# Kernel optimization log

Measured on AMD Instinct MI355X. Metric: run time of the kernel, lower is better.

The kernel has to match this reference:

```python
import jax, jax.numpy as jnp
import numpy as np

EPS = 1e-5
N_NODES = 10
NUM_JOINTS = 6   # all robot_configs fixed to '3_segments_3DOF' (module's fallback default)
MAX_DOF = 10


def _lin(x, w, b):
    # torch nn.Linear: y = x @ W.T + b, W is (out, in)
    return jnp.einsum('...i,oi->...o', x, w) + b


def _layernorm(x, scale, bias):
    mu = x.mean(-1, keepdims=True)
    var = x.var(-1, keepdims=True)
    return (x - mu) / jnp.sqrt(var + EPS) * scale + bias


def _forward(images, text_lengths, node_features, edge_indices, p):
    B = images.shape[0]
    # --- SimplifiedVLMBackbone ---
    y = jax.lax.conv_general_dilated(images, p['conv_w'], (2, 2), [(3, 3), (3, 3)],
                                     dimension_numbers=('NCHW', 'OIHW', 'NCHW'))
    y = jax.nn.relu(y + p['conv_b'][None, :, None, None])          # (B,32,112,112)
    y = y.reshape(B, 32, 7, 16, 7, 16).mean(axis=(3, 5))            # adaptive avg pool -> (B,32,7,7)
    y = y.reshape(B, 32 * 49)
    y = jax.nn.relu(_lin(y, p['img_fc1_w'], p['img_fc1_b']))
    img_feat = _lin(y, p['img_fc2_w'], p['img_fc2_b'])               # (B,768)
    t = p['text_emb'][jnp.clip(text_lengths, 0, 9999)]               # (B,256)
    vlm = img_feat + _lin(t, p['text_fc_w'], p['text_fc_b'])         # (B,768)

    # --- SoftArmGraphNN ---
    x = jax.nn.relu(_lin(node_features, p['enc1_w'], p['enc1_b']))
    x = _lin(x, p['enc2_w'], p['enc2_b'])                            # (B,N,64)
    src, dst = edge_indices[:, 0, :], edge_indices[:, 1, :]          # (B,E)

    def agg_fn(xi, si, di):
        # mean of neighbor (source) features per destination node; 0 if no neighbors
        g = xi[si]                                                   # (E,D)
        s = jax.ops.segment_sum(g, di, num_segments=N_NODES)
        c = jax.ops.segment_sum(jnp.ones(di.shape, xi.dtype), di, num_segments=N_NODES)
        return s / jnp.maximum(c, 1.0)[:, None]

    for i in range(3):
        residual = x
        mean_nb = jax.vmap(agg_fn)(x, src, dst)                      # (B,N,64)
        comb = jnp.concatenate([x, mean_nb], axis=-1)                # (B,N,128)
        x = _lin(comb, p['gc_w'][i], p['gc_b'][i])
        x = jax.nn.relu(_layernorm(x + residual, p['ln_scale'][i], p['ln_bias'][i]))
    graph_tokens = _lin(x, p['proj_w'], p['proj_b'])                 # (B,N,32)

    # --- AttentionPooling + dual-path fusion ---
    s = _lin(jnp.tanh(_lin(graph_tokens, p['attn1_w'], p['attn1_b'])), p['attn2_w'], p['attn2_b'])
    w = jax.nn.softmax(s, axis=1)                                    # (B,N,1)
    robot_token = jnp.sum(graph_tokens * w, axis=1)                  # (B,32) -> project? 32 vs 768 -> residual add via broadcast pad
    fused = vlm.at[:, :robot_token.shape[-1]].add(robot_token)       # global token residual into vlm features

    # --- NodeActionHead (all samples: 3seg_3DOF -> 6 joints, per-joint MLPs) ---
    comb = jnp.concatenate([
        jnp.broadcast_to(fused[:, None, :], (B, NUM_JOINTS, fused.shape[-1])),
        graph_tokens[:, :NUM_JOINTS, :]], axis=-1)                   # (B,J,800)
    h = jax.nn.relu(jnp.einsum('bjf,jhf->bjh', comb, p['head_w1']) + p['head_b1'])
    h = jax.nn.relu(jnp.einsum('bjf,jhf->bjh', h, p['head_w2']) + p['head_b2'])
    a = jnp.einsum('bjf,jhf->bjh', h, p['head_w3']) + p['head_b3']   # (B,6,16)
    a = jnp.pad(a, ((0, 0), (0, MAX_DOF - NUM_JOINTS), (0, 0)))      # pad to max_dof
    return jnp.transpose(a, (0, 2, 1))                               # (B,16,10)


def setup_inputs() -> dict:
    key = jax.random.key(0)
    ks = iter(jax.random.split(key, 64))

    def nrm(shape, scale=0.02):
        return scale * jax.random.normal(next(ks), shape, dtype=jnp.float32)

    B = 128
    inp = {
        'images': jax.random.normal(next(ks), (B, 3, 224, 224), dtype=jnp.float32),
        'text_lengths': jax.random.randint(next(ks), (B,), 0, 10000, dtype=jnp.int32),
        'node_features': jax.random.normal(next(ks), (B, N_NODES, 19), dtype=jnp.float32),
        'edge_indices': jax.random.randint(next(ks), (B, 2, 18), 0, N_NODES, dtype=jnp.int32),
        'conv_w': nrm((32, 3, 7, 7)), 'conv_b': jnp.zeros(32, jnp.float32),
        'img_fc1_w': nrm((512, 1568)), 'img_fc1_b': jnp.zeros(512, jnp.float32),
        'img_fc2_w': nrm((768, 512)), 'img_fc2_b': jnp.zeros(768, jnp.float32),
        'text_emb': nrm((10000, 256)),
        'text_fc_w': nrm((768, 256)), 'text_fc_b': jnp.zeros(768, jnp.float32),
        'enc1_w': nrm((64, 19)), 'enc1_b': jnp.zeros(64, jnp.float32),
        'enc2_w': nrm((64, 64)), 'enc2_b': jnp.zeros(64, jnp.float32),
        'gc_w': nrm((3, 64, 128)), 'gc_b': jnp.zeros((3, 64), jnp.float32),
        'ln_scale': jnp.ones((3, 64), jnp.float32), 'ln_bias': jnp.zeros((3, 64), jnp.float32),
        'proj_w': nrm((32, 64)), 'proj_b': jnp.zeros(32, jnp.float32),
        'attn1_w': nrm((16, 32)), 'attn1_b': jnp.zeros(16, jnp.float32),
        'attn2_w': nrm((1, 16)), 'attn2_b': jnp.zeros(1, jnp.float32),
        'head_w1': nrm((6, 128, 800)), 'head_b1': jnp.zeros((6, 128), jnp.float32),
        'head_w2': nrm((6, 64, 128)), 'head_b2': jnp.zeros((6, 64), jnp.float32),
        'head_w3': nrm((6, 16, 64)), 'head_b3': jnp.zeros((6, 16), jnp.float32),
    }
    return inp


def reference(images, text_lengths, node_features, edge_indices, conv_w, conv_b,
              img_fc1_w, img_fc1_b, img_fc2_w, img_fc2_b, text_emb, text_fc_w, text_fc_b,
              enc1_w, enc1_b, enc2_w, enc2_b, gc_w, gc_b, ln_scale, ln_bias,
              proj_w, proj_b, attn1_w, attn1_b, attn2_w, attn2_b,
              head_w1, head_b1, head_w2, head_b2, head_w3, head_b3):
    p = dict(conv_w=conv_w, conv_b=conv_b, img_fc1_w=img_fc1_w, img_fc1_b=img_fc1_b,
             img_fc2_w=img_fc2_w, img_fc2_b=img_fc2_b, text_emb=text_emb,
             text_fc_w=text_fc_w, text_fc_b=text_fc_b, enc1_w=enc1_w, enc1_b=enc1_b,
             enc2_w=enc2_w, enc2_b=enc2_b, gc_w=gc_w, gc_b=gc_b, ln_scale=ln_scale,
             ln_bias=ln_bias, proj_w=proj_w, proj_b=proj_b, attn1_w=attn1_w,
             attn1_b=attn1_b, attn2_w=attn2_w, attn2_b=attn2_b, head_w1=head_w1,
             head_b1=head_b1, head_w2=head_w2, head_b2=head_b2, head_w3=head_w3,
             head_b3=head_b3)
    return _forward(images, text_lengths, node_features, edge_indices, p)
```

## Files before the change

kernel.cpp:

```cpp
#include <hip/hip_runtime.h>
#include <hip/hip_bf16.h>
#include <math.h>

typedef __attribute__((ext_vector_type(8))) short bf16x8;
typedef __attribute__((ext_vector_type(4))) float f32x4;

static __device__ __forceinline__ unsigned short f2bf(float f) {
    union { float f; unsigned int u; } x{f};
    unsigned int u = x.u;
    unsigned int r = (u + 0x7fffu + ((u >> 16) & 1u)) >> 16;
    return (unsigned short)r;
}

static __device__ __forceinline__ unsigned int pack2(float f0, float f1) {
    __hip_bfloat162 h = __float22bfloat162_rn(float2{f0, f1});
    union { __hip_bfloat162 h; unsigned int u; } c{h};
    return c.u;
}

__global__ __launch_bounds__(256) void wprep(const float* __restrict__ conv_w,
                                             unsigned short* __restrict__ wB) {
    for (int idx = threadIdx.x; idx < 24 * 32 * 8; idx += 256) {
        int s = idx >> 8;
        int ch = (idx >> 3) & 31;
        int kx = idx & 7;
        int c = s >> 3, ky = s & 7;
        float v = 0.f;
        if (ky < 7 && kx < 7) v = conv_w[ch * 147 + c * 49 + ky * 7 + kx];
        wB[idx] = f2bf(v);
    }
}

#define PSTRIDE 120
__global__ __launch_bounds__(512, 4) void conv_mfma(const float* __restrict__ img,
                                                    const unsigned int* __restrict__ wBu,
                                                    const float* __restrict__ cb,
                                                    float* __restrict__ pooled) {
    __shared__ unsigned int patch[111 * PSTRIDE];
    const int t = threadIdx.x;
    const int py = blockIdx.x, b = blockIdx.y;
    const int lane = t & 63, wid = t >> 6;
    const int r16 = lane & 15, g = lane >> 4;
    const int Y0 = 32 * py - 3;

    const int xc0 = 2 * lane - 3;
    const int xc1 = 2 * lane + 125;
    const int a00 = max(xc0, 0);
    const int a01 = max(xc0 + 1, 0);
    const int a10 = min(xc1, 223);
    const int a11 = min(xc1 + 1, 223);
    const bool v00 = (xc0 >= 0);
    const bool v01 = (xc0 + 1 >= 0);
    const bool v10 = (xc1 <= 223);
    const bool v11 = (xc1 + 1 <= 223);
    const bool c1act = (lane < 52);

    const float* ib = img + (size_t)b * 3 * 224 * 224;

#pragma unroll
    for (int hb = 0; hb < 2; ++hb) {
        float g0[7], g1[7], g2[7], g3[7];
        int rr[7];
        bool rv[7];
        const float* rp[7];
#pragma unroll
        for (int i = 0; i < 7; ++i) {
            int r = wid + 8 * (hb * 7 + i);
            int c_ = (r >= 74) ? 2 : ((r >= 37) ? 1 : 0);
            int pr = r - 37 * c_;
            int iy = Y0 + pr;
            rv[i] = (r < 111) & (iy >= 0) & (iy < 224);
            int iyc = min(max(iy, 0), 223);
            rp[i] = ib + (c_ * 224 + iyc) * 224;
            rr[i] = r;
            g0[i] = rp[i][a00];
            g1[i] = rp[i][a01];
            g2[i] = rp[i][a10];
            g3[i] = rp[i][a11];
        }
#pragma unroll
        for (int i = 0; i < 7; ++i) {
            float f0 = (rv[i] && v00) ? g0[i] : 0.f;
            float f1 = (rv[i] && v01) ? g1[i] : 0.f;
            float f2_ = (rv[i] && v10) ? g2[i] : 0.f;
            float f3 = (rv[i] && v11) ? g3[i] : 0.f;
            if (rr[i] < 111) {
                patch[rr[i] * PSTRIDE + lane] = pack2(f0, f1);
                if (c1act) patch[rr[i] * PSTRIDE + 64 + lane] = pack2(f2_, f3);
            }
        }
    }

    bf16x8 bfrA[6], bfrB[6];
    int rowoff[6];
#pragma unroll
    for (int k = 0; k < 6; ++k) {
        int s = 4 * k + g;
        int c = s >> 3, ky = s & 7;
        int kyc = ky > 6 ? 6 : ky;
        rowoff[k] = c * 37 + kyc;
        union { uint4 q; bf16x8 v; } ua, ub;
        ua.q = *(const uint4*)(wBu + (s * 32 + r16) * 4);
        ub.q = *(const uint4*)(wBu + (s * 32 + r16 + 16) * 4);
        bfrA[k] = ua.v;
        bfrB[k] = ub.v;
    }
    const float biasA = cb[r16], biasB = cb[r16 + 16];

    __syncthreads();

    float accA[7], accB[7];
#pragma unroll
    for (int p = 0; p < 7; ++p) accA[p] = accB[p] = 0.f;

#pragma unroll
    for (int q = 0; q < 2; ++q) {
        const int oyl = 2 * wid + q;
        int rb[6];
#pragma unroll
        for (int k = 0; k < 6; ++k) rb[k] = (rowoff[k] + 2 * oyl) * PSTRIDE;

        for (int t7 = 0; t7 < 7; ++t7) {
            const int oxr = 16 * t7 + r16;
            f32x4 C0 = {biasA, biasA, biasA, biasA};
            f32x4 C1 = {biasB, biasB, biasB, biasB};
#pragma unroll
            for (int k = 0; k < 6; ++k) {
                const unsigned int* ap = &patch[rb[k] + oxr];
                union { unsigned int u[4]; bf16x8 v; } ua;
                ua.u[0] = ap[0];
                ua.u[1] = ap[1];
                ua.u[2] = ap[2];
                ua.u[3] = ap[3];
                C0 = __builtin_amdgcn_mfma_f32_16x16x32_bf16(ua.v, bfrA[k], C0, 0, 0, 0);
                C1 = __builtin_amdgcn_mfma_f32_16x16x32_bf16(ua.v, bfrB[k], C1, 0, 0, 0);
            }
            float s0 = 0.f, s1 = 0.f;
#pragma unroll
            for (int r = 0; r < 4; ++r) {
                s0 += fmaxf(C0[r], 0.f);
                s1 += fmaxf(C1[r], 0.f);
            }
            accA[t7] += s0;
            accB[t7] += s1;
        }
    }
#pragma unroll
    for (int p = 0; p < 7; ++p) {
        accA[p] += __shfl_xor(accA[p], 16);
        accA[p] += __shfl_xor(accA[p], 32);
        accB[p] += __shfl_xor(accB[p], 16);
        accB[p] += __shfl_xor(accB[p], 32);
    }
    __syncthreads();
    float* sw = (float*)patch;
    if (lane < 16) {
#pragma unroll
        for (int p = 0; p < 7; ++p) {
            sw[(wid * 7 + p) * 32 + lane] = accA[p];
            sw[(wid * 7 + p) * 32 + lane + 16] = accB[p];
        }
    }
    __syncthreads();
    if (t < 224) {
        int p = t >> 5, ch = t & 31;
        float s = 0.f;
#pragma unroll
        for (int w = 0; w < 8; ++w) s += sw[(w * 7 + p) * 32 + ch];
        pooled[(size_t)b * 1568 + ch * 49 + py * 7 + p] = s * (1.f / 256.f);
    }
}

__global__ __launch_bounds__(256) void fc1_k(const float* __restrict__ in,
                                             const float* __restrict__ w,
                                             const float* __restrict__ bias,
                                             float* __restrict__ out) {
    __shared__ __align__(16) float xsm[8][1568];
    const int t = threadIdx.x;
    const int lane = t & 63, wid = t >> 6;
    const int ob = blockIdx.x & 31;
    const int bg = blockIdx.x >> 5;
    const int b0 = bg * 8;

#pragma unroll
    for (int r = 0; r < 8; ++r)
        for (int i = t; i < 392; i += 256)
            *(float4*)&xsm[r][i * 4] = *(const float4*)(in + (size_t)(b0 + r) * 1568 + i * 4);
    __syncthreads();

#pragma unroll
    for (int oi = 0; oi < 4; ++oi) {
        const int o = ob * 16 + oi * 4 + wid;
        const float4* wr = (const float4*)(w + (size_t)o * 1568);
        float acc[8] = {0, 0, 0, 0, 0, 0, 0, 0};
        for (int i = lane; i < 392; i += 64) {
            float4 wv = wr[i];
#pragma unroll
            for (int r = 0; r < 8; ++r) {
                float4 xv = *(const float4*)&xsm[r][i * 4];
                acc[r] = fmaf(xv.x, wv.x, acc[r]);
                acc[r] = fmaf(xv.y, wv.y, acc[r]);
                acc[r] = fmaf(xv.z, wv.z, acc[r]);
                acc[r] = fmaf(xv.w, wv.w, acc[r]);
            }
        }
#pragma unroll
        for (int r = 0; r < 8; ++r) {
            acc[r] += __shfl_xor(acc[r], 32);
            acc[r] += __shfl_xor(acc[r], 16);
            acc[r] += __shfl_xor(acc[r], 8);
            acc[r] += __shfl_xor(acc[r], 4);
            acc[r] += __shfl_xor(acc[r], 2);
            acc[r] += __shfl_xor(acc[r], 1);
        }
        float v = 0.f;
#pragma unroll
        for (int r = 0; r < 8; ++r)
            if (lane == r) v = acc[r];
        if (lane < 8) out[(size_t)(b0 + lane) * 512 + o] = fmaxf(v + bias[o], 0.f);
    }
}

__global__ __launch_bounds__(256) void vlm_k(const float* __restrict__ h1,
                                             const float* __restrict__ w2,
                                             const float* __restrict__ b2,
                                             const int* __restrict__ tlen,
                                             const float* __restrict__ temb,
                                             const float* __restrict__ tw,
                                             const float* __restrict__ tb,
                                             const float* __restrict__ rtok,
                                             float* __restrict__ fused) {
    __shared__ __align__(16) float xs1[8][512];
    __shared__ __align__(16) float xst[8][256];
    __shared__ int srow[8];
    const int t = threadIdx.x;
    const int lane = t & 63, wid = t >> 6;
    const int ob = blockIdx.x % 24;
    const int bg = blockIdx.x / 24;
    const int b0 = bg * 8;

    if (t < 8) {
        int r = tlen[b0 + t];
        srow[t] = min(max(r, 0), 9999);
    }
#pragma unroll
    for (int rr = 0; rr < 4; ++rr) {
        int r = rr * 2 + (t >> 7);
        int i = t & 127;
        *(float4*)&xs1[r][i * 4] = *(const float4*)(h1 + (size_t)(b0 + r) * 512 + i * 4);
    }
    __syncthreads();
#pragma unroll
    for (int rr = 0; rr < 2; ++rr) {
        int r = rr * 4 + (t >> 6);
        int i = t & 63;
        *(float4*)&xst[r][i * 4] = *(const float4*)(temb + (size_t)srow[r] * 256 + i * 4);
    }
    __syncthreads();

#pragma unroll
    for (int oi = 0; oi < 8; ++oi) {
        const int o = ob * 32 + oi * 4 + wid;
        float acc[8] = {0, 0, 0, 0, 0, 0, 0, 0};
        {
            const float4* wr = (const float4*)(w2 + (size_t)o * 512);
#pragma unroll
            for (int ii = 0; ii < 2; ++ii) {
                int i = lane + ii * 64;
                float4 wv = wr[i];
#pragma unroll
                for (int r = 0; r < 8; ++r) {
                    float4 xv = *(const float4*)&xs1[r][i * 4];
                    acc[r] = fmaf(xv.x, wv.x, acc[r]);
                    acc[r] = fmaf(xv.y, wv.y, acc[r]);
                    acc[r] = fmaf(xv.z, wv.z, acc[r]);
                    acc[r] = fmaf(xv.w, wv.w, acc[r]);
                }
            }
        }
        {
            const float4* wt4 = (const float4*)(tw + (size_t)o * 256);
            float4 wv = wt4[lane];
#pragma unroll
            for (int r = 0; r < 8; ++r) {
                float4 xv = *(const float4*)&xst[r][lane * 4];
                acc[r] = fmaf(xv.x, wv.x, acc[r]);
                acc[r] = fmaf(xv.y, wv.y, acc[r]);
                acc[r] = fmaf(xv.z, wv.z, acc[r]);
                acc[r] = fmaf(xv.w, wv.w, acc[r]);
            }
        }
#pragma unroll
        for (int r = 0; r < 8; ++r) {
            acc[r] += __shfl_xor(acc[r], 32);
            acc[r] += __shfl_xor(acc[r], 16);
            acc[r] += __shfl_xor(acc[r], 8);
            acc[r] += __shfl_xor(acc[r], 4);
            acc[r] += __shfl_xor(acc[r], 2);
            acc[r] += __shfl_xor(acc[r], 1);
        }
        float v = 0.f;
#pragma unroll
        for (int r = 0; r < 8; ++r)
            if (lane == r) v = acc[r];
        if (lane < 8) {
            float add = (o < 32) ? rtok[(size_t)(b0 + lane) * 32 + o] : 0.f;
            fused[(size_t)(b0 + lane) * 768 + o] = v + b2[o] + tb[o] + add;
        }
    }
}

__global__ __launch_bounds__(640, 1) void graph_k(
    const float* __restrict__ nfeat, const int* __restrict__ eidx,
    const float* __restrict__ e1w, const float* __restrict__ e1b,
    const float* __restrict__ e2w, const float* __restrict__ e2b,
    const float* __restrict__ gcw, const float* __restrict__ gcb,
    const float* __restrict__ lns, const float* __restrict__ lnb,
    const float* __restrict__ pjw, const float* __restrict__ pjb,
    const float* __restrict__ a1w, const float* __restrict__ a1b,
    const float* __restrict__ a2w, const float* __restrict__ a2b,
    float* __restrict__ gts_g, float* __restrict__ rtok) {
    __shared__ __align__(16) float pool[8448];
    __shared__ __align__(16) float nf[10][20];
    __shared__ __align__(16) float xsA[10][64];
    __shared__ __align__(16) float xsB[10][64];
    __shared__ __align__(16) float nbs[10][64];
    __shared__ __align__(16) float gtss[10][32];
    __shared__ float svs[10];
    __shared__ int se[18], de[18];
    const int t = threadIdx.x;
    const int b = blockIdx.x;
    const int n = t >> 6, o = t & 63;

    if (t < 190) {
        int nn = t / 19, i = t - nn * 19;
        nf[nn][i] = nfeat[(size_t)(b * 10 + nn) * 19 + i];
    }
    if (t < 36) {
        if (t < 18) se[t] = eidx[b * 36 + t];
        else de[t - 18] = eidx[b * 36 + t];
    }
    float* e1wT = pool;
    float* e2wT = pool + 1280;
    for (int u = t; u < 1216; u += 640) {
        int oo = u / 19, k = u - oo * 19;
        e1wT[k * 64 + oo] = e1w[u];
    }
    for (int u = t; u < 4096; u += 640) {
        int oo = u >> 6, k = u & 63;
        e2wT[k * 65 + oo] = e2w[u];
    }
    __syncthreads();

    {
        float acc = e1b[o];
#pragma unroll
        for (int i = 0; i < 19; ++i) acc = fmaf(nf[n][i], e1wT[i * 64 + o], acc);
        xsB[n][o] = fmaxf(acc, 0.f);
    }
    {
        const float* xrow = &xsB[n][0];
        float s0 = 0, s1 = 0, s2 = 0, s3 = 0;
#pragma unroll
        for (int k = 0; k < 64; k += 4) {
            s0 = fmaf(xrow[k], e2wT[k * 65 + o], s0);
            s1 = fmaf(xrow[k + 1], e2wT[(k + 1) * 65 + o], s1);
            s2 = fmaf(xrow[k + 2], e2wT[(k + 2) * 65 + o], s2);
            s3 = fmaf(xrow[k + 3], e2wT[(k + 3) * 65 + o], s3);
        }
        xsA[n][o] = e2b[o] + ((s0 + s1) + (s2 + s3));
    }
    __syncthreads();

    float* src = &xsA[0][0];
    float* dst = &xsB[0][0];
    for (int l = 0; l < 3; ++l) {
        const float* gl = gcw + (size_t)l * 8192;
        for (int u = t; u < 8192; u += 640) {
            int oo = u >> 7, k = u & 127;
            pool[k * 65 + oo] = gl[u];
        }
        {
            float s = 0.f;
            int cnt = 0;
#pragma unroll
            for (int e = 0; e < 18; ++e) {
                bool m = (de[e] == n);
                float v = src[se[e] * 64 + o];
                s += m ? v : 0.f;
                cnt += m ? 1 : 0;
            }
            nbs[n][o] = s / (float)(cnt > 1 ? cnt : 1);
        }
        __syncthreads();
        {
            const float* xa = src + n * 64;
            const float* xb = &nbs[n][0];
            float s0 = 0, s1 = 0, s2 = 0, s3 = 0;
#pragma unroll
            for (int k = 0; k < 64; k += 4) {
                s0 = fmaf(xa[k], pool[k * 65 + o], s0);
                s1 = fmaf(xa[k + 1], pool[(k + 1) * 65 + o], s1);
                s2 = fmaf(xa[k + 2], pool[(k + 2) * 65 + o], s2);
                s3 = fmaf(xa[k + 3], pool[(k + 3) * 65 + o], s3);
            }
#pragma unroll
            for (int k = 0; k < 64; k += 4) {
                s0 = fmaf(xb[k], pool[(64 + k) * 65 + o], s0);
                s1 = fmaf(xb[k + 1], pool[(64 + k + 1) * 65 + o], s1);
                s2 = fmaf(xb[k + 2], pool[(64 + k + 2) * 65 + o], s2);
                s3 = fmaf(xb[k + 3], pool[(64 + k + 3) * 65 + o], s3);
            }
            float v = gcb[l * 64 + o] + ((s0 + s1) + (s2 + s3)) + xa[o];
            float mu = v;
            mu += __shfl_xor(mu, 32);
            mu += __shfl_xor(mu, 16);
            mu += __shfl_xor(mu, 8);
            mu += __shfl_xor(mu, 4);
            mu += __shfl_xor(mu, 2);
            mu += __shfl_xor(mu, 1);
            mu *= (1.f / 64.f);
            float d = v - mu;
            float vr = d * d;
            vr += __shfl_xor(vr, 32);
            vr += __shfl_xor(vr, 16);
            vr += __shfl_xor(vr, 8);
            vr += __shfl_xor(vr, 4);
            vr += __shfl_xor(vr, 2);
            vr += __shfl_xor(vr, 1);
            vr *= (1.f / 64.f);
            dst[n * 64 + o] =
                fmaxf(d / sqrtf(vr + 1e-5f) * lns[l * 64 + o] + lnb[l * 64 + o], 0.f);
        }
        __syncthreads();
        float* tmp = src;
        src = dst;
        dst = tmp;
    }

    float* pjwT = pool;
    float* a1wT = pool + 2112;
    for (int u = t; u < 2048; u += 640) {
        int oo = u >> 6, k = u & 63;
        pjwT[k * 33 + oo] = pjw[u];
    }
    for (int u = t; u < 512; u += 640) {
        int hh = u >> 5, k = u & 31;
        a1wT[k * 17 + hh] = a1w[u];
    }
    __syncthreads();

    if (o < 32) {
        const float* xrow = src + n * 64;
        float s0 = 0, s1 = 0, s2 = 0, s3 = 0;
#pragma unroll
        for (int k = 0; k < 64; k += 4) {
            s0 = fmaf(xrow[k], pjwT[k * 33 + o], s0);
            s1 = fmaf(xrow[k + 1], pjwT[(k + 1) * 33 + o], s1);
            s2 = fmaf(xrow[k + 2], pjwT[(k + 2) * 33 + o], s2);
            s3 = fmaf(xrow[k + 3], pjwT[(k + 3) * 33 + o], s3);
        }
        float gv = pjb[o] + ((s0 + s1) + (s2 + s3));
        gtss[n][o] = gv;
        gts_g[(size_t)b * 320 + n * 32 + o] = gv;
    }
    if (o < 16) {
        const float* xrow = &gtss[n][0];
        float s0 = 0, s1 = 0, s2 = 0, s3 = 0;
#pragma unroll
        for (int k = 0; k < 32; k += 4) {
            s0 = fmaf(xrow[k], a1wT[k * 17 + o], s0);
            s1 = fmaf(xrow[k + 1], a1wT[(k + 1) * 17 + o], s1);
            s2 = fmaf(xrow[k + 2], a1wT[(k + 2) * 17 + o], s2);
            s3 = fmaf(xrow[k + 3], a1wT[(k + 3) * 17 + o], s3);
        }
        float z = a1b[o] + ((s0 + s1) + (s2 + s3));
        float sc = tanhf(z) * a2w[o];
        sc += __shfl_xor(sc, 8);
        sc += __shfl_xor(sc, 4);
        sc += __shfl_xor(sc, 2);
        sc += __shfl_xor(sc, 1);
        if (o == 0) svs[n] = sc + a2b[0];
    }
    __syncthreads();

    if (n == 0 && o < 32) {
        float m = svs[0];
#pragma unroll
        for (int i = 1; i < 10; ++i) m = fmaxf(m, svs[i]);
        float e[10];
        float sum = 0.f;
#pragma unroll
        for (int i = 0; i < 10; ++i) {
            e[i] = expf(svs[i] - m);
            sum += e[i];
        }
        float inv = 1.f / sum;
        float rt = 0.f;
#pragma unroll
        for (int nn = 0; nn < 10; ++nn) rt = fmaf(gtss[nn][o], e[nn] * inv, rt);
        rtok[(size_t)b * 32 + o] = rt;
    }
}

__global__ __launch_bounds__(256) void head1_k(const float* __restrict__ fused,
                                               const float* __restrict__ gts,
                                               const float* __restrict__ w1,
                                               const float* __restrict__ b1,
                                               float* __restrict__ h1T) {
    __shared__ __align__(16) float xsm[8][800];
    const int t = threadIdx.x;
    const int ob = blockIdx.x % 24;
    const int bg = blockIdx.x / 24;
    const int b0 = bg * 8;
    const int j = ob >> 2;
    const int lane = t & 63, wid = t >> 6;

    for (int u = t; u < 1600; u += 256) {
        int row = u / 200, i = u - row * 200;
        float4 v;
        if (i < 192)
            v = *(const float4*)(fused + (size_t)(b0 + row) * 768 + i * 4);
        else
            v = *(const float4*)(gts + (size_t)(b0 + row) * 320 + j * 32 + (i - 192) * 4);
        *(float4*)&xsm[row][i * 4] = v;
    }
    __syncthreads();

#pragma unroll
    for (int oi = 0; oi < 8; ++oi) {
        const int o = ob * 32 + oi * 4 + wid;
        const float4* wr = (const float4*)(w1 + (size_t)o * 800);
        float acc[8] = {0, 0, 0, 0, 0, 0, 0, 0};
        for (int i = lane; i < 200; i += 64) {
            float4 wv = wr[i];
#pragma unroll
            for (int r = 0; r < 8; ++r) {
                float4 xv = *(const float4*)&xsm[r][i * 4];
                acc[r] = fmaf(xv.x, wv.x, acc[r]);
                acc[r] = fmaf(xv.y, wv.y, acc[r]);
                acc[r] = fmaf(xv.z, wv.z, acc[r]);
                acc[r] = fmaf(xv.w, wv.w, acc[r]);
            }
        }
#pragma unroll
        for (int r = 0; r < 8; ++r) {
            acc[r] += __shfl_xor(acc[r], 32);
            acc[r] += __shfl_xor(acc[r], 16);
            acc[r] += __shfl_xor(acc[r], 8);
            acc[r] += __shfl_xor(acc[r], 4);
            acc[r] += __shfl_xor(acc[r], 2);
            acc[r] += __shfl_xor(acc[r], 1);
        }
        float v = 0.f;
#pragma unroll
        for (int r = 0; r < 8; ++r)
            if (lane == r) v = acc[r];
        if (lane < 8) h1T[(size_t)o * 128 + b0 + lane] = fmaxf(v + b1[o], 0.f);
    }
}

__global__ __launch_bounds__(128) void head2_k(const float* __restrict__ h1T,
                                               const float* __restrict__ w2,
                                               const float* __restrict__ b2,
                                               float* __restrict__ h2T) {
    const int o2 = blockIdx.x;
    const int j = o2 >> 6;
    const int b = threadIdx.x;
    const float* wrow = w2 + (size_t)o2 * 128;
    const float* xcol = h1T + (size_t)j * 128 * 128 + b;
    float acc = b2[o2];
#pragma unroll 16
    for (int k = 0; k < 128; ++k) acc = fmaf(xcol[k * 128], wrow[k], acc);
    h2T[(size_t)o2 * 128 + b] = fmaxf(acc, 0.f);
}

__global__ __launch_bounds__(128) void head3_k(const float* __restrict__ h2T,
                                               const float* __restrict__ w3,
                                               const float* __restrict__ b3,
                                               float* __restrict__ out) {
    const int jj = blockIdx.x % 10;
    const int oo = blockIdx.x / 10;
    const int b = threadIdx.x;
    float acc = 0.f;
    if (jj < 6) {
        const float* wrow = w3 + (size_t)(jj * 16 + oo) * 64;
        const float* xcol = h2T + (size_t)jj * 64 * 128 + b;
        acc = b3[jj * 16 + oo];
#pragma unroll 16
        for (int k = 0; k < 64; ++k) acc = fmaf(xcol[k * 128], wrow[k], acc);
    }
    out[(size_t)b * 160 + oo * 10 + jj] = acc;
}

extern "C" void kernel_launch(void* const* d_in, const int* in_sizes, int n_in,
                              void* d_out, int out_size, void* d_ws, size_t ws_size,
                              hipStream_t stream) {
    const float* images = (const float*)d_in[0];
    const int* tlen = (const int*)d_in[1];
    const float* nfeat = (const float*)d_in[2];
    const int* eidx = (const int*)d_in[3];
    const float* conv_w = (const float*)d_in[4];
    const float* conv_b = (const float*)d_in[5];
    const float* fc1w = (const float*)d_in[6];
    const float* fc1b = (const float*)d_in[7];
    const float* fc2w = (const float*)d_in[8];
    const float* fc2b = (const float*)d_in[9];
    const float* temb = (const float*)d_in[10];
    const float* tfw = (const float*)d_in[11];
    const float* tfb = (const float*)d_in[12];
    const float* e1w = (const float*)d_in[13];
    const float* e1b = (const float*)d_in[14];
    const float* e2w = (const float*)d_in[15];
    const float* e2b = (const float*)d_in[16];
    const float* gcw = (const float*)d_in[17];
    const float* gcb = (const float*)d_in[18];
    const float* lns = (const float*)d_in[19];
    const float* lnb = (const float*)d_in[20];
    const float* pjw = (const float*)d_in[21];
    const float* pjb = (const float*)d_in[22];
    const float* a1w = (const float*)d_in[23];
    const float* a1b = (const float*)d_in[24];
    const float* a2w = (const float*)d_in[25];
    const float* a2b = (const float*)d_in[26];
    const float* w1 = (const float*)d_in[27];
    const float* b1 = (const float*)d_in[28];
    const float* w2 = (const float*)d_in[29];
    const float* b2 = (const float*)d_in[30];
    const float* w3 = (const float*)d_in[31];
    const float* b3 = (const float*)d_in[32];

    const int B = in_sizes[0] / (3 * 224 * 224);

    float* ws = (float*)d_ws;
    unsigned short* wB = (unsigned short*)d_ws;
    float* pooled = ws + 3072;
    float* h1fc = pooled + (size_t)B * 1568;
    float* fused = h1fc + (size_t)B * 512;
    float* gts = fused + (size_t)B * 768;
    float* rtok = gts + (size_t)B * 320;
    float* h1T = pooled;
    float* h2T = pooled + 98304;

    wprep<<<1, 256, 0, stream>>>(conv_w, wB);
    conv_mfma<<<dim3(7, B), 512, 0, stream>>>(images, (const unsigned int*)wB,
                                              conv_b, pooled);
    fc1_k<<<32 * 16, 256, 0, stream>>>(pooled, fc1w, fc1b, h1fc);
    graph_k<<<B, 640, 0, stream>>>(nfeat, eidx, e1w, e1b, e2w, e2b, gcw, gcb,
                                   lns, lnb, pjw, pjb, a1w, a1b, a2w, a2b,
                                   gts, rtok);
    vlm_k<<<24 * 16, 256, 0, stream>>>(h1fc, fc2w, fc2b, tlen, temb, tfw, tfb,
                                       rtok, fused);
    head1_k<<<24 * 16, 256, 0, stream>>>(fused, gts, w1, b1, h1T);
    head2_k<<<384, 128, 0, stream>>>(h1T, w2, b2, h2T);
    head3_k<<<160, 128, 0, stream>>>(h2T, w3, b3, (float*)d_out);
}
```

Baseline: 136.2 us.

## Split conv blocks by row half and register-block FC kernels without shared staging

The convolution grid is doubled by splitting each pooled row band into two halves, which shrinks shared memory per block and raises the occupancy hint. Each half writes its own partial pooled buffer, and fc1 sums the two when it reads its input. fc1, vlm and head1 drop their shared-memory staging: each wave now computes 4 outputs per pass, reading activations straight from global memory and reusing them across those outputs, and vlm/head1 launch twice as many blocks. This trades more redundant global or L2 activation reads for more parallelism and no barriers.

```diff
diff --git a/kernel.cpp b/kernel.cpp
--- a/kernel.cpp
+++ b/kernel.cpp
@@ -32,16 +32,17 @@
 }
 
 #define PSTRIDE 120
-__global__ __launch_bounds__(512, 4) void conv_mfma(const float* __restrict__ img,
+__global__ __launch_bounds__(512, 6) void conv_mfma(const float* __restrict__ img,
                                                     const unsigned int* __restrict__ wBu,
                                                     const float* __restrict__ cb,
-                                                    float* __restrict__ pooled) {
-    __shared__ unsigned int patch[111 * PSTRIDE];
+                                                    float* __restrict__ pooledH) {
+    __shared__ unsigned int patch[63 * PSTRIDE];
     const int t = threadIdx.x;
-    const int py = blockIdx.x, b = blockIdx.y;
+    const int py = blockIdx.x, half = blockIdx.y, b = blockIdx.z;
+    const int B = gridDim.z;
     const int lane = t & 63, wid = t >> 6;
     const int r16 = lane & 15, g = lane >> 4;
-    const int Y0 = 32 * py - 3;
+    const int Y0 = 32 * py + 16 * half - 3;
 
     const int xc0 = 2 * lane - 3;
     const int xc1 = 2 * lane + 125;
@@ -59,32 +60,31 @@
 
 #pragma unroll
     for (int hb = 0; hb < 2; ++hb) {
-        float g0[7], g1[7], g2[7], g3[7];
-        int rr[7];
-        bool rv[7];
-        const float* rp[7];
-#pragma unroll
-        for (int i = 0; i < 7; ++i) {
-            int r = wid + 8 * (hb * 7 + i);
-            int c_ = (r >= 74) ? 2 : ((r >= 37) ? 1 : 0);
-            int pr = r - 37 * c_;
+        float g0[4], g1[4], g2[4], g3[4];
+        int rr[4];
+        bool rv[4];
+#pragma unroll
+        for (int i = 0; i < 4; ++i) {
+            int r = wid + 8 * (hb * 4 + i);
+            int c_ = (r >= 42) ? 2 : ((r >= 21) ? 1 : 0);
+            int pr = r - 21 * c_;
             int iy = Y0 + pr;
-            rv[i] = (r < 111) & (iy >= 0) & (iy < 224);
+            rv[i] = (r < 63) & (iy >= 0) & (iy < 224);
             int iyc = min(max(iy, 0), 223);
-            rp[i] = ib + (c_ * 224 + iyc) * 224;
+            const float* rp = ib + (c_ * 224 + iyc) * 224;
             rr[i] = r;
-            g0[i] = rp[i][a00];
-            g1[i] = rp[i][a01];
-            g2[i] = rp[i][a10];
-            g3[i] = rp[i][a11];
-        }
-#pragma unroll
-        for (int i = 0; i < 7; ++i) {
+            g0[i] = rp[a00];
+            g1[i] = rp[a01];
+            g2[i] = rp[a10];
+            g3[i] = rp[a11];
+        }
+#pragma unroll
+        for (int i = 0; i < 4; ++i) {
             float f0 = (rv[i] && v00) ? g0[i] : 0.f;
             float f1 = (rv[i] && v01) ? g1[i] : 0.f;
             float f2_ = (rv[i] && v10) ? g2[i] : 0.f;
             float f3 = (rv[i] && v11) ? g3[i] : 0.f;
-            if (rr[i] < 111) {
+            if (rr[i] < 63) {
                 patch[rr[i] * PSTRIDE + lane] = pack2(f0, f1);
                 if (c1act) patch[rr[i] * PSTRIDE + 64 + lane] = pack2(f2_, f3);
             }
@@ -98,7 +98,7 @@
         int s = 4 * k + g;
         int c = s >> 3, ky = s & 7;
         int kyc = ky > 6 ? 6 : ky;
-        rowoff[k] = c * 37 + kyc;
+        rowoff[k] = c * 21 + kyc;
         union { uint4 q; bf16x8 v; } ua, ub;
         ua.q = *(const uint4*)(wBu + (s * 32 + r16) * 4);
         ub.q = *(const uint4*)(wBu + (s * 32 + r16 + 16) * 4);
@@ -110,40 +110,33 @@
     __syncthreads();
 
     float accA[7], accB[7];
-#pragma unroll
-    for (int p = 0; p < 7; ++p) accA[p] = accB[p] = 0.f;
-
-#pragma unroll
-    for (int q = 0; q < 2; ++q) {
-        const int oyl = 2 * wid + q;
-        int rb[6];
-#pragma unroll
-        for (int k = 0; k < 6; ++k) rb[k] = (rowoff[k] + 2 * oyl) * PSTRIDE;
-
-        for (int t7 = 0; t7 < 7; ++t7) {
-            const int oxr = 16 * t7 + r16;
-            f32x4 C0 = {biasA, biasA, biasA, biasA};
-            f32x4 C1 = {biasB, biasB, biasB, biasB};
-#pragma unroll
-            for (int k = 0; k < 6; ++k) {
-                const unsigned int* ap = &patch[rb[k] + oxr];
-                union { unsigned int u[4]; bf16x8 v; } ua;
-                ua.u[0] = ap[0];
-                ua.u[1] = ap[1];
-                ua.u[2] = ap[2];
-                ua.u[3] = ap[3];
-                C0 = __builtin_amdgcn_mfma_f32_16x16x32_bf16(ua.v, bfrA[k], C0, 0, 0, 0);
-                C1 = __builtin_amdgcn_mfma_f32_16x16x32_bf16(ua.v, bfrB[k], C1, 0, 0, 0);
-            }
-            float s0 = 0.f, s1 = 0.f;
-#pragma unroll
-            for (int r = 0; r < 4; ++r) {
-                s0 += fmaxf(C0[r], 0.f);
-                s1 += fmaxf(C1[r], 0.f);
-            }
-            accA[t7] += s0;
-            accB[t7] += s1;
-        }
+    int rb[6];
+#pragma unroll
+    for (int k = 0; k < 6; ++k) rb[k] = (rowoff[k] + 2 * wid) * PSTRIDE;
+
+    for (int t7 = 0; t7 < 7; ++t7) {
+        const int oxr = 16 * t7 + r16;
+        f32x4 C0 = {biasA, biasA, biasA, biasA};
+        f32x4 C1 = {biasB, biasB, biasB, biasB};
+#pragma unroll
+        for (int k = 0; k < 6; ++k) {
+            const unsigned int* ap = &patch[rb[k] + oxr];
+            union { unsigned int u[4]; bf16x8 v; } ua;
+            ua.u[0] = ap[0];
+            ua.u[1] = ap[1];
+            ua.u[2] = ap[2];
+            ua.u[3] = ap[3];
+            C0 = __builtin_amdgcn_mfma_f32_16x16x32_bf16(ua.v, bfrA[k], C0, 0, 0, 0);
+            C1 = __builtin_amdgcn_mfma_f32_16x16x32_bf16(ua.v, bfrB[k], C1, 0, 0, 0);
+        }
+        float s0 = 0.f, s1 = 0.f;
+#pragma unroll
+        for (int r = 0; r < 4; ++r) {
+            s0 += fmaxf(C0[r], 0.f);
+            s1 += fmaxf(C1[r], 0.f);
+        }
+        accA[t7] = s0;
+        accB[t7] = s1;
     }
 #pragma unroll
     for (int p = 0; p < 7; ++p) {
@@ -167,57 +160,63 @@
         float s = 0.f;
 #pragma unroll
         for (int w = 0; w < 8; ++w) s += sw[(w * 7 + p) * 32 + ch];
-        pooled[(size_t)b * 1568 + ch * 49 + py * 7 + p] = s * (1.f / 256.f);
+        pooledH[(size_t)(half * B + b) * 1568 + ch * 49 + py * 7 + p] = s * (1.f / 256.f);
     }
 }
 
 __global__ __launch_bounds__(256) void fc1_k(const float* __restrict__ in,
                                              const float* __restrict__ w,
                                              const float* __restrict__ bias,
-                                             float* __restrict__ out) {
-    __shared__ __align__(16) float xsm[8][1568];
-    const int t = threadIdx.x;
-    const int lane = t & 63, wid = t >> 6;
-    const int ob = blockIdx.x & 31;
+                                             float* __restrict__ out, int B) {
+    const int t = threadIdx.x, lane = t & 63, wid = t >> 6;
+    const int qg = blockIdx.x & 31;
     const int bg = blockIdx.x >> 5;
     const int b0 = bg * 8;
-
-#pragma unroll
-    for (int r = 0; r < 8; ++r)
-        for (int i = t; i < 392; i += 256)
-            *(float4*)&xsm[r][i * 4] = *(const float4*)(in + (size_t)(b0 + r) * 1568 + i * 4);
-    __syncthreads();
-
-#pragma unroll
-    for (int oi = 0; oi < 4; ++oi) {
-        const int o = ob * 16 + oi * 4 + wid;
-        const float4* wr = (const float4*)(w + (size_t)o * 1568);
-        float acc[8] = {0, 0, 0, 0, 0, 0, 0, 0};
-        for (int i = lane; i < 392; i += 64) {
-            float4 wv = wr[i];
-#pragma unroll
-            for (int r = 0; r < 8; ++r) {
-                float4 xv = *(const float4*)&xsm[r][i * 4];
-                acc[r] = fmaf(xv.x, wv.x, acc[r]);
-                acc[r] = fmaf(xv.y, wv.y, acc[r]);
-                acc[r] = fmaf(xv.z, wv.z, acc[r]);
-                acc[r] = fmaf(xv.w, wv.w, acc[r]);
-            }
-        }
+    const int o0 = (qg * 4 + wid) * 4;
+    const float4* wp = (const float4*)w;
+    const float4* xp0 = (const float4*)in;
+    const float4* xp1 = xp0 + (size_t)B * 392;
+
+    float acc[4][8];
+#pragma unroll
+    for (int oo = 0; oo < 4; ++oo)
+#pragma unroll
+        for (int r = 0; r < 8; ++r) acc[oo][r] = 0.f;
+
+    for (int i = lane; i < 392; i += 64) {
+        float4 wv[4];
+#pragma unroll
+        for (int oo = 0; oo < 4; ++oo) wv[oo] = wp[(size_t)(o0 + oo) * 392 + i];
 #pragma unroll
         for (int r = 0; r < 8; ++r) {
-            acc[r] += __shfl_xor(acc[r], 32);
-            acc[r] += __shfl_xor(acc[r], 16);
-            acc[r] += __shfl_xor(acc[r], 8);
-            acc[r] += __shfl_xor(acc[r], 4);
-            acc[r] += __shfl_xor(acc[r], 2);
-            acc[r] += __shfl_xor(acc[r], 1);
-        }
+            float4 a = xp0[(size_t)(b0 + r) * 392 + i];
+            float4 c = xp1[(size_t)(b0 + r) * 392 + i];
+            float4 xv = {a.x + c.x, a.y + c.y, a.z + c.z, a.w + c.w};
+#pragma unroll
+            for (int oo = 0; oo < 4; ++oo) {
+                acc[oo][r] = fmaf(xv.x, wv[oo].x, acc[oo][r]);
+                acc[oo][r] = fmaf(xv.y, wv[oo].y, acc[oo][r]);
+                acc[oo][r] = fmaf(xv.z, wv[oo].z, acc[oo][r]);
+                acc[oo][r] = fmaf(xv.w, wv[oo].w, acc[oo][r]);
+            }
+        }
+    }
+#pragma unroll
+    for (int oo = 0; oo < 4; ++oo) {
         float v = 0.f;
 #pragma unroll
-        for (int r = 0; r < 8; ++r)
-            if (lane == r) v = acc[r];
-        if (lane < 8) out[(size_t)(b0 + lane) * 512 + o] = fmaxf(v + bias[o], 0.f);
+        for (int r = 0; r < 8; ++r) {
+            float s = acc[oo][r];
+            s += __shfl_xor(s, 32);
+            s += __shfl_xor(s, 16);
+            s += __shfl_xor(s, 8);
+            s += __shfl_xor(s, 4);
+            s += __shfl_xor(s, 2);
+            s += __shfl_xor(s, 1);
+            if (lane == r) v = s;
+        }
+        if (lane < 8)
+            out[(size_t)(b0 + lane) * 512 + o0 + oo] = fmaxf(v + bias[o0 + oo], 0.f);
     }
 }
 
@@ -230,79 +229,78 @@
                                              const float* __restrict__ tb,
                                              const float* __restrict__ rtok,
                                              float* __restrict__ fused) {
-    __shared__ __align__(16) float xs1[8][512];
-    __shared__ __align__(16) float xst[8][256];
-    __shared__ int srow[8];
-    const int t = threadIdx.x;
-    const int lane = t & 63, wid = t >> 6;
-    const int ob = blockIdx.x % 24;
-    const int bg = blockIdx.x / 24;
+    const int t = threadIdx.x, lane = t & 63, wid = t >> 6;
+    const int ogq = blockIdx.x % 48;
+    const int bg = blockIdx.x / 48;
     const int b0 = bg * 8;
-
-    if (t < 8) {
-        int r = tlen[b0 + t];
-        srow[t] = min(max(r, 0), 9999);
-    }
-#pragma unroll
-    for (int rr = 0; rr < 4; ++rr) {
-        int r = rr * 2 + (t >> 7);
-        int i = t & 127;
-        *(float4*)&xs1[r][i * 4] = *(const float4*)(h1 + (size_t)(b0 + r) * 512 + i * 4);
-    }
-    __syncthreads();
-#pragma unroll
-    for (int rr = 0; rr < 2; ++rr) {
-        int r = rr * 4 + (t >> 6);
-        int i = t & 63;
-        *(float4*)&xst[r][i * 4] = *(const float4*)(temb + (size_t)srow[r] * 256 + i * 4);
-    }
-    __syncthreads();
-
-#pragma unroll
-    for (int oi = 0; oi < 8; ++oi) {
-        const int o = ob * 32 + oi * 4 + wid;
-        float acc[8] = {0, 0, 0, 0, 0, 0, 0, 0};
-        {
-            const float4* wr = (const float4*)(w2 + (size_t)o * 512);
-#pragma unroll
-            for (int ii = 0; ii < 2; ++ii) {
-                int i = lane + ii * 64;
-                float4 wv = wr[i];
-#pragma unroll
-                for (int r = 0; r < 8; ++r) {
-                    float4 xv = *(const float4*)&xs1[r][i * 4];
-                    acc[r] = fmaf(xv.x, wv.x, acc[r]);
-                    acc[r] = fmaf(xv.y, wv.y, acc[r]);
-                    acc[r] = fmaf(xv.z, wv.z, acc[r]);
-                    acc[r] = fmaf(xv.w, wv.w, acc[r]);
-                }
-            }
-        }
-        {
-            const float4* wt4 = (const float4*)(tw + (size_t)o * 256);
-            float4 wv = wt4[lane];
-#pragma unroll
-            for (int r = 0; r < 8; ++r) {
-                float4 xv = *(const float4*)&xst[r][lane * 4];
-                acc[r] = fmaf(xv.x, wv.x, acc[r]);
-                acc[r] = fmaf(xv.y, wv.y, acc[r]);
-                acc[r] = fmaf(xv.z, wv.z, acc[r]);
-                acc[r] = fmaf(xv.w, wv.w, acc[r]);
-            }
-        }
+    const int o0 = (ogq * 4 + wid) * 4;
+
+    int rows[8];
+#pragma unroll
+    for (int r = 0; r < 8; ++r) {
+        int v = tlen[b0 + r];
+        rows[r] = min(max(v, 0), 9999);
+    }
+    const float4* wp = (const float4*)w2;
+    const float4* xp = (const float4*)h1;
+    const float4* wtp = (const float4*)tw;
+    const float4* xtp = (const float4*)temb;
+
+    float acc[4][8];
+#pragma unroll
+    for (int oo = 0; oo < 4; ++oo)
+#pragma unroll
+        for (int r = 0; r < 8; ++r) acc[oo][r] = 0.f;
+
+#pragma unroll
+    for (int ii = 0; ii < 2; ++ii) {
+        int i = lane + (ii << 6);
+        float4 wv[4];
+#pragma unroll
+        for (int oo = 0; oo < 4; ++oo) wv[oo] = wp[(size_t)(o0 + oo) * 128 + i];
 #pragma unroll
         for (int r = 0; r < 8; ++r) {
-            acc[r] += __shfl_xor(acc[r], 32);
-            acc[r] += __shfl_xor(acc[r], 16);
-            acc[r] += __shfl_xor(acc[r], 8);
-            acc[r] += __shfl_xor(acc[r], 4);
-            acc[r] += __shfl_xor(acc[r], 2);
-            acc[r] += __shfl_xor(acc[r], 1);
-        }
+            float4 xv = xp[(size_t)(b0 + r) * 128 + i];
+#pragma unroll
+            for (int oo = 0; oo < 4; ++oo) {
+                acc[oo][r] = fmaf(xv.x, wv[oo].x, acc[oo][r]);
+                acc[oo][r] = fmaf(xv.y, wv[oo].y, acc[oo][r]);
+                acc[oo][r] = fmaf(xv.z, wv[oo].z, acc[oo][r]);
+                acc[oo][r] = fmaf(xv.w, wv[oo].w, acc[oo][r]);
+            }
+        }
+    }
+    {
+        float4 wv[4];
+#pragma unroll
+        for (int oo = 0; oo < 4; ++oo) wv[oo] = wtp[(size_t)(o0 + oo) * 64 + lane];
+#pragma unroll
+        for (int r = 0; r < 8; ++r) {
+            float4 xv = xtp[(size_t)rows[r] * 64 + lane];
+#pragma unroll
+            for (int oo = 0; oo < 4; ++oo) {
+                acc[oo][r] = fmaf(xv.x, wv[oo].x, acc[oo][r]);
+                acc[oo][r] = fmaf(xv.y, wv[oo].y, acc[oo][r]);
+                acc[oo][r] = fmaf(xv.z, wv[oo].z, acc[oo][r]);
+                acc[oo][r] = fmaf(xv.w, wv[oo].w, acc[oo][r]);
+            }
+        }
+    }
+#pragma unroll
+    for (int oo = 0; oo < 4; ++oo) {
         float v = 0.f;
 #pragma unroll
-        for (int r = 0; r < 8; ++r)
-            if (lane == r) v = acc[r];
+        for (int r = 0; r < 8; ++r) {
+            float s = acc[oo][r];
+            s += __shfl_xor(s, 32);
+            s += __shfl_xor(s, 16);
+            s += __shfl_xor(s, 8);
+            s += __shfl_xor(s, 4);
+            s += __shfl_xor(s, 2);
+            s += __shfl_xor(s, 1);
+            if (lane == r) v = s;
+        }
+        int o = o0 + oo;
         if (lane < 8) {
             float add = (o < 32) ? rtok[(size_t)(b0 + lane) * 32 + o] : 0.f;
             fused[(size_t)(b0 + lane) * 768 + o] = v + b2[o] + tb[o] + add;
@@ -508,54 +506,54 @@
                                                const float* __restrict__ w1,
                                                const float* __restrict__ b1,
                                                float* __restrict__ h1T) {
-    __shared__ __align__(16) float xsm[8][800];
-    const int t = threadIdx.x;
-    const int ob = blockIdx.x % 24;
-    const int bg = blockIdx.x / 24;
+    const int t = threadIdx.x, lane = t & 63, wid = t >> 6;
+    const int ogq = blockIdx.x % 48;
+    const int bg = blockIdx.x / 48;
     const int b0 = bg * 8;
-    const int j = ob >> 2;
-    const int lane = t & 63, wid = t >> 6;
-
-    for (int u = t; u < 1600; u += 256) {
-        int row = u / 200, i = u - row * 200;
-        float4 v;
-        if (i < 192)
-            v = *(const float4*)(fused + (size_t)(b0 + row) * 768 + i * 4);
-        else
-            v = *(const float4*)(gts + (size_t)(b0 + row) * 320 + j * 32 + (i - 192) * 4);
-        *(float4*)&xsm[row][i * 4] = v;
-    }
-    __syncthreads();
-
-#pragma unroll
-    for (int oi = 0; oi < 8; ++oi) {
-        const int o = ob * 32 + oi * 4 + wid;
-        const float4* wr = (const float4*)(w1 + (size_t)o * 800);
-        float acc[8] = {0, 0, 0, 0, 0, 0, 0, 0};
-        for (int i = lane; i < 200; i += 64) {
-            float4 wv = wr[i];
-#pragma unroll
-            for (int r = 0; r < 8; ++r) {
-                float4 xv = *(const float4*)&xsm[r][i * 4];
-                acc[r] = fmaf(xv.x, wv.x, acc[r]);
-                acc[r] = fmaf(xv.y, wv.y, acc[r]);
-                acc[r] = fmaf(xv.z, wv.z, acc[r]);
-                acc[r] = fmaf(xv.w, wv.w, acc[r]);
-            }
-        }
+    const int j = ogq >> 3;
+    const int o0 = ogq * 16 + wid * 4;
+    const float4* wp = (const float4*)w1;
+    const float4* fp = (const float4*)fused;
+    const float4* gp = (const float4*)gts;
+
+    float acc[4][8];
+#pragma unroll
+    for (int oo = 0; oo < 4; ++oo)
+#pragma unroll
+        for (int r = 0; r < 8; ++r) acc[oo][r] = 0.f;
+
+    for (int i = lane; i < 200; i += 64) {
+        float4 wv[4];
+#pragma unroll
+        for (int oo = 0; oo < 4; ++oo) wv[oo] = wp[(size_t)(o0 + oo) * 200 + i];
 #pragma unroll
         for (int r = 0; r < 8; ++r) {
-            acc[r] += __shfl_xor(acc[r], 32);
-            acc[r] += __shfl_xor(acc[r], 16);
-            acc[r] += __shfl_xor(acc[r], 8);
-            acc[r] += __shfl_xor(acc[r], 4);
-            acc[r] += __shfl_xor(acc[r], 2);
-            acc[r] += __shfl_xor(acc[r], 1);
-        }
+            float4 xv = (i < 192) ? fp[(size_t)(b0 + r) * 192 + i]
+                                  : gp[(size_t)(b0 + r) * 80 + j * 8 + (i - 192)];
+#pragma unroll
+            for (int oo = 0; oo < 4; ++oo) {
+                acc[oo][r] = fmaf(xv.x, wv[oo].x, acc[oo][r]);
+                acc[oo][r] = fmaf(xv.y, wv[oo].y, acc[oo][r]);
+                acc[oo][r] = fmaf(xv.z, wv[oo].z, acc[oo][r]);
+                acc[oo][r] = fmaf(xv.w, wv[oo].w, acc[oo][r]);
+            }
+        }
+    }
+#pragma unroll
+    for (int oo = 0; oo < 4; ++oo) {
         float v = 0.f;
 #pragma unroll
-        for (int r = 0; r < 8; ++r)
-            if (lane == r) v = acc[r];
+        for (int r = 0; r < 8; ++r) {
+            float s = acc[oo][r];
+            s += __shfl_xor(s, 32);
+            s += __shfl_xor(s, 16);
+            s += __shfl_xor(s, 8);
+            s += __shfl_xor(s, 4);
+            s += __shfl_xor(s, 2);
+            s += __shfl_xor(s, 1);
+            if (lane == r) v = s;
+        }
+        int o = o0 + oo;
         if (lane < 8) h1T[(size_t)o * 128 + b0 + lane] = fmaxf(v + b1[o], 0.f);
     }
 }
@@ -634,24 +632,24 @@
 
     float* ws = (float*)d_ws;
     unsigned short* wB = (unsigned short*)d_ws;
-    float* pooled = ws + 3072;
-    float* h1fc = pooled + (size_t)B * 1568;
+    float* pooledH = ws + 3072;
+    float* h1fc = pooledH + (size_t)2 * B * 1568;
     float* fused = h1fc + (size_t)B * 512;
     float* gts = fused + (size_t)B * 768;
     float* rtok = gts + (size_t)B * 320;
-    float* h1T = pooled;
-    float* h2T = pooled + 98304;
+    float* h1T = pooledH;
+    float* h2T = pooledH + 98304;
 
     wprep<<<1, 256, 0, stream>>>(conv_w, wB);
-    conv_mfma<<<dim3(7, B), 512, 0, stream>>>(images, (const unsigned int*)wB,
-                                              conv_b, pooled);
-    fc1_k<<<32 * 16, 256, 0, stream>>>(pooled, fc1w, fc1b, h1fc);
+    conv_mfma<<<dim3(7, 2, B), 512, 0, stream>>>(images, (const unsigned int*)wB,
+                                                 conv_b, pooledH);
+    fc1_k<<<512, 256, 0, stream>>>(pooledH, fc1w, fc1b, h1fc, B);
     graph_k<<<B, 640, 0, stream>>>(nfeat, eidx, e1w, e1b, e2w, e2b, gcw, gcb,
                                    lns, lnb, pjw, pjb, a1w, a1b, a2w, a2b,
                                    gts, rtok);
-    vlm_k<<<24 * 16, 256, 0, stream>>>(h1fc, fc2w, fc2b, tlen, temb, tfw, tfb,
-                                       rtok, fused);
-    head1_k<<<24 * 16, 256, 0, stream>>>(fused, gts, w1, b1, h1T);
+    vlm_k<<<768, 256, 0, stream>>>(h1fc, fc2w, fc2b, tlen, temb, tfw, tfb,
+                                   rtok, fused);
+    head1_k<<<768, 256, 0, stream>>>(fused, gts, w1, b1, h1T);
     head2_k<<<384, 128, 0, stream>>>(h1T, w2, b2, h2T);
     head3_k<<<160, 128, 0, stream>>>(h2T, w3, b3, (float*)d_out);
 }
```

Measured after the change: 163.5 us. 20.0% more time.
